# Optimization experiments

Hardware: AMD Instinct MI355X
Metric: run time of the kernel (lower is better)

## Reference

```python
import jax, jax.numpy as jnp
import numpy as np

B, L, D, H, F = 4, 1024, 1024, 16, 4096
HD = D // H
EPS = 1e-5


def _xavier(key, shape):
    fan_in, fan_out = shape[1], shape[0]
    a = np.sqrt(6.0 / (fan_in + fan_out)).astype(np.float32)
    return jax.random.uniform(key, shape, jnp.float32, -a, a)


def setup_inputs() -> dict:
    key = jax.random.key(0)
    ks = jax.random.split(key, 8)
    x = jax.random.normal(ks[0], (B, L, D), jnp.float32)
    attn_mask = jnp.zeros((L, L), jnp.float32)
    return {
        "x": x,
        "attn_mask": attn_mask,
        "in_proj_w": _xavier(ks[1], (3 * D, D)),
        "in_proj_b": jnp.zeros((3 * D,), jnp.float32),
        "out_proj_w": _xavier(ks[2], (D, D)),
        "out_proj_b": jnp.zeros((D,), jnp.float32),
        "lin1_w": _xavier(ks[3], (F, D)),
        "lin1_b": jnp.zeros((F,), jnp.float32),
        "lin2_w": _xavier(ks[4], (D, F)),
        "lin2_b": jnp.zeros((D,), jnp.float32),
        "ln1_g": jnp.ones((D,), jnp.float32),
        "ln1_b": jnp.zeros((D,), jnp.float32),
        "ln2_g": jnp.ones((D,), jnp.float32),
        "ln2_b": jnp.zeros((D,), jnp.float32),
    }


def _layernorm(x, g, b):
    mu = jnp.mean(x, axis=-1, keepdims=True)
    var = jnp.mean(jnp.square(x - mu), axis=-1, keepdims=True)
    return (x - mu) * jax.lax.rsqrt(var + EPS) * g + b


def reference(x, attn_mask, in_proj_w, in_proj_b, out_proj_w, out_proj_b,
              lin1_w, lin1_b, lin2_w, lin2_b, ln1_g, ln1_b, ln2_g, ln2_b):
    # --- self-attention (need_weights=True, average_attn_weights=False) ---
    qkv = x @ in_proj_w.T + in_proj_b          # [B,L,3D]
    q, k, v = jnp.split(qkv, 3, axis=-1)
    q = q.reshape(B, L, H, HD).transpose(0, 2, 1, 3)  # [B,H,L,hd]
    k = k.reshape(B, L, H, HD).transpose(0, 2, 1, 3)
    v = v.reshape(B, L, H, HD).transpose(0, 2, 1, 3)
    scores = jnp.einsum('bhqd,bhkd->bhqk', q, k) / np.sqrt(HD).astype(np.float32)
    scores = scores + attn_mask                # additive [L,L] mask
    attn_w = jax.nn.softmax(scores, axis=-1)   # [B,H,L,L] materialized weights
    ctx = jnp.einsum('bhqk,bhkd->bhqd', attn_w, v)
    ctx = ctx.transpose(0, 2, 1, 3).reshape(B, L, D)
    attn_out = ctx @ out_proj_w.T + out_proj_b
    # --- norm_first=False residual blocks ---
    x = _layernorm(x + attn_out, ln1_g, ln1_b)
    ff = jax.nn.relu(x @ lin1_w.T + lin1_b) @ lin2_w.T + lin2_b
    x = _layernorm(x + ff, ln2_g, ln2_b)
    return (x, attn_w)
```

## Files before the change

### kernel.cpp

```cpp
#include <hip/hip_runtime.h>

#define Bq 4
#define Lq 1024
#define Dq 1024
#define Hq 16
#define HDq 64
#define Fq 4096
#define Mq (Bq*Lq)

typedef unsigned short u16;
using short8  = __attribute__((ext_vector_type(8))) short;
using floatx4 = __attribute__((ext_vector_type(4))) float;

__device__ __forceinline__ float b2f(u16 u) {
  union { unsigned int i; float f; } v; v.i = ((unsigned int)u) << 16; return v.f;
}
__device__ __forceinline__ u16 f2b(float f) {
  union { float f; unsigned int i; } v; v.f = f;
  unsigned int x = v.i;
  unsigned int r = x + 0x7fffu + ((x >> 16) & 1u);
  return (u16)(r >> 16);
}

__device__ __forceinline__ void split2(float v, u16& hi, u16& lo) {
  hi = f2b(v);
  lo = f2b(v - b2f(hi));
}

__device__ __forceinline__ void gl_lds16(const u16* g, u16* l) {
  __builtin_amdgcn_global_load_lds(
      (const __attribute__((address_space(1))) void*)g,
      (__attribute__((address_space(3))) void*)l, 16, 0, 0);
}

__launch_bounds__(256)
__global__ void cvt_f32_bf16(const float* __restrict__ s, u16* __restrict__ d, int n4) {
  const int i = (blockIdx.x * 256 + threadIdx.x) * 4;
  if (i < n4) {
    float4 v = *(const float4*)(s + i);
    ushort4 o;
    o.x = f2b(v.x); o.y = f2b(v.y); o.z = f2b(v.z); o.w = f2b(v.w);
    *(ushort4*)(d + i) = o;
  }
}

template<bool RELU, typename OutT>
__launch_bounds__(256)
__global__ void gemm_bt(const u16* __restrict__ A, int lda,
                        const u16* __restrict__ B, int ldb,
                        const float* __restrict__ bias,
                        OutT* __restrict__ C, int ldc,
                        int K) {
  __shared__ __align__(16) u16 As[128 * 32];
  __shared__ __align__(16) u16 Bs[128 * 32];
  const int tid  = threadIdx.x;
  const int m0   = blockIdx.y * 128;
  const int n0   = blockIdx.x * 128;
  const int lane = tid & 63;
  const int wave = tid >> 6;
  const int wm   = (wave >> 1) * 64;
  const int wn   = (wave & 1) * 64;
  const int lrow = lane & 15;
  const int lk   = (lane >> 4) * 8;

  const int c0 = tid, c1 = tid + 256;
  const int ar0 = c0 >> 2, ac0 = (c0 & 3) * 8;
  const int ar1 = c1 >> 2, ac1 = (c1 & 3) * 8;

  floatx4 acc[4][4] = {};

  for (int k0 = 0; k0 < K; k0 += 32) {
    gl_lds16(A + (size_t)(m0 + ar0) * lda + k0 + ac0, &As[c0 * 8]);
    gl_lds16(A + (size_t)(m0 + ar1) * lda + k0 + ac1, &As[c1 * 8]);
    gl_lds16(B + (size_t)(n0 + ar0) * ldb + k0 + ac0, &Bs[c0 * 8]);
    gl_lds16(B + (size_t)(n0 + ar1) * ldb + k0 + ac1, &Bs[c1 * 8]);
    __syncthreads();

    short8 af[4], bf[4];
#pragma unroll
    for (int t = 0; t < 4; ++t) {
      af[t] = *(const short8*)&As[(wm + t * 16 + lrow) * 32 + lk];
      bf[t] = *(const short8*)&Bs[(wn + t * 16 + lrow) * 32 + lk];
    }
#pragma unroll
    for (int i = 0; i < 4; ++i)
#pragma unroll
      for (int j = 0; j < 4; ++j)
        acc[i][j] = __builtin_amdgcn_mfma_f32_16x16x32_bf16(af[i], bf[j], acc[i][j], 0, 0, 0);
    __syncthreads();
  }

#pragma unroll
  for (int i = 0; i < 4; ++i) {
    const int row = m0 + wm + i * 16 + (lane >> 4) * 4;
#pragma unroll
    for (int j = 0; j < 4; ++j) {
      const int col = n0 + wn + j * 16 + lrow;
      const float bv = bias[col];
#pragma unroll
      for (int r = 0; r < 4; ++r) {
        float v = acc[i][j][r] + bv;
        if (RELU) v = v > 0.f ? v : 0.f;
        if constexpr (sizeof(OutT) == 4) C[(size_t)(row + r) * ldc + col] = v;
        else                             C[(size_t)(row + r) * ldc + col] = f2b(v);
      }
    }
  }
}

__launch_bounds__(256)
__global__ void transpose_v(const float* __restrict__ qkv, u16* __restrict__ vt) {
  __shared__ __align__(16) float t[64][65];
  const int kt = blockIdx.x;
  const int h  = blockIdx.y;
  const int b  = blockIdx.z;
  const int tid = threadIdx.x;
#pragma unroll
  for (int i = 0; i < 16; ++i) {
    int e = i * 256 + tid;
    int kk = e >> 6, d = e & 63;
    t[kk][d] = qkv[((size_t)(b * Lq + kt * 64 + kk)) * (3 * Dq) + 2 * Dq + h * HDq + d];
  }
  __syncthreads();
#pragma unroll
  for (int i = 0; i < 16; ++i) {
    int e = i * 256 + tid;
    int drow = e >> 6, kcol = e & 63;
    vt[(((size_t)(b * Hq + h)) * HDq + drow) * Lq + kt * 64 + kcol] = f2b(t[kcol][drow]);
  }
}

__launch_bounds__(256)
__global__ void split_k(const float* __restrict__ qkv,
                        u16* __restrict__ kh, u16* __restrict__ kl) {
  const int gid = blockIdx.x * 256 + threadIdx.x;
  const int oct = gid & 7;
  const int l   = (gid >> 3) & 1023;
  const int h   = (gid >> 13) & 15;
  const int b   = gid >> 17;
  const float* src = qkv + ((size_t)(b * Lq + l)) * (3 * Dq) + Dq + h * HDq + oct * 8;
  float4 a = *(const float4*)src;
  float4 c = *(const float4*)(src + 4);
  float v[8] = {a.x, a.y, a.z, a.w, c.x, c.y, c.z, c.w};
  short8 hi, lo;
#pragma unroll
  for (int j = 0; j < 8; ++j) {
    u16 hh, ll; split2(v[j], hh, ll);
    hi[j] = (short)hh; lo[j] = (short)ll;
  }
  const size_t off = (((size_t)(b * Hq + h)) * Lq + l) * HDq + oct * 8;
  *(short8*)(kh + off) = hi;
  *(short8*)(kl + off) = lo;
}

__device__ __forceinline__ int ps_idx(int row, int col) {
  return row * 1024 + ((((col >> 3) ^ (row & 7)) << 3) | (col & 7));
}

__device__ __forceinline__ void load_split8(const float* p, short8& hi, short8& lo) {
  float4 a = *(const float4*)p;
  float4 b = *(const float4*)(p + 4);
  float v[8] = {a.x, a.y, a.z, a.w, b.x, b.y, b.z, b.w};
#pragma unroll
  for (int j = 0; j < 8; ++j) {
    u16 h, l; split2(v[j], h, l);
    hi[j] = (short)h; lo[j] = (short)l;
  }
}

__launch_bounds__(512, 4)
__global__ void attn_kernel(const float* __restrict__ qkv,
                            const u16* __restrict__ kh,
                            const u16* __restrict__ kl,
                            const u16* __restrict__ vt,
                            const float* __restrict__ mask,
                            float* __restrict__ attn_w,
                            u16* __restrict__ ctx) {
  __shared__ __align__(16) u16 Ps[16 * 1024];
  __shared__ float redmax[8][16];
  __shared__ float redsum[8][16];
  __shared__ float Pp[4][16][17];

  int lid = (int)blockIdx.x + ((int)blockIdx.y << 6) + ((int)blockIdx.z << 10);
  lid = (lid & 7) * 512 + (lid >> 3);
  const int qt = lid & 63, h = (lid >> 6) & 15, b = lid >> 10;
  const int bh = b * Hq + h;
  const int tid  = threadIdx.x;
  const int lane = tid & 63, wave = tid >> 6;
  const int lrow = lane & 15, quad = lane >> 4;
  const int q0 = qt * 16;

  const float* qbase = qkv + ((size_t)(b * Lq + q0 + lrow)) * (3 * Dq) + h * HDq + quad * 8;
  short8 aqh0, aql0, aqh1, aql1;
  load_split8(qbase,      aqh0, aql0);
  load_split8(qbase + 32, aqh1, aql1);

  const u16* khb = kh + ((size_t)bh * Lq) * HDq + quad * 8;
  const u16* klb = kl + ((size_t)bh * Lq) * HDq + quad * 8;
  floatx4 sc[8];
#pragma unroll
  for (int i = 0; i < 8; ++i) {
    const int n0 = wave * 128 + i * 16;
    const u16* kbh = khb + (size_t)(n0 + lrow) * HDq;
    const u16* kbl = klb + (size_t)(n0 + lrow) * HDq;
    short8 k0h = *(const short8*)kbh;
    short8 k1h = *(const short8*)(kbh + 32);
    short8 k0l = *(const short8*)kbl;
    short8 k1l = *(const short8*)(kbl + 32);
    floatx4 s = {};
    s = __builtin_amdgcn_mfma_f32_16x16x32_bf16(aqh0, k0h, s, 0, 0, 0);
    s = __builtin_amdgcn_mfma_f32_16x16x32_bf16(aqh0, k0l, s, 0, 0, 0);
    s = __builtin_amdgcn_mfma_f32_16x16x32_bf16(aql0, k0h, s, 0, 0, 0);
    s = __builtin_amdgcn_mfma_f32_16x16x32_bf16(aqh1, k1h, s, 0, 0, 0);
    s = __builtin_amdgcn_mfma_f32_16x16x32_bf16(aqh1, k1l, s, 0, 0, 0);
    s = __builtin_amdgcn_mfma_f32_16x16x32_bf16(aql1, k1h, s, 0, 0, 0);
    sc[i] = s;
  }

  const float* mbase = mask + (size_t)(q0 + quad * 4) * Lq + wave * 128 + lrow;
  float mx[4] = {-1e30f, -1e30f, -1e30f, -1e30f};
#pragma unroll
  for (int i = 0; i < 8; ++i)
#pragma unroll
    for (int r = 0; r < 4; ++r) {
      float v = sc[i][r] * 0.125f + mbase[(size_t)r * Lq + i * 16];
      sc[i][r] = v;
      mx[r] = fmaxf(mx[r], v);
    }
#pragma unroll
  for (int s = 1; s < 16; s <<= 1)
#pragma unroll
    for (int r = 0; r < 4; ++r) mx[r] = fmaxf(mx[r], __shfl_xor(mx[r], s, 16));
  if (lrow == 0) {
#pragma unroll
    for (int r = 0; r < 4; ++r) redmax[wave][quad * 4 + r] = mx[r];
  }
  __syncthreads();
  float M[4];
#pragma unroll
  for (int r = 0; r < 4; ++r) {
    float m = redmax[0][quad * 4 + r];
#pragma unroll
    for (int w = 1; w < 8; ++w) m = fmaxf(m, redmax[w][quad * 4 + r]);
    M[r] = m;
  }

  float sm[4] = {0.f, 0.f, 0.f, 0.f};
#pragma unroll
  for (int i = 0; i < 8; ++i)
#pragma unroll
    for (int r = 0; r < 4; ++r) {
      float p = __expf(sc[i][r] - M[r]);
      sc[i][r] = p;
      sm[r] += p;
    }
#pragma unroll
  for (int s = 1; s < 16; s <<= 1)
#pragma unroll
    for (int r = 0; r < 4; ++r) sm[r] += __shfl_xor(sm[r], s, 16);
  if (lrow == 0) {
#pragma unroll
    for (int r = 0; r < 4; ++r) redsum[wave][quad * 4 + r] = sm[r];
  }
  __syncthreads();
  float scl[4];
#pragma unroll
  for (int r = 0; r < 4; ++r) {
    float t = redsum[0][quad * 4 + r];
#pragma unroll
    for (int w = 1; w < 8; ++w) t += redsum[w][quad * 4 + r];
    scl[r] = 1.f / t;
  }

  float* wbase = attn_w + ((size_t)bh * Lq + q0 + quad * 4) * Lq + wave * 128 + lrow;
#pragma unroll
  for (int i = 0; i < 8; ++i)
#pragma unroll
    for (int r = 0; r < 4; ++r) {
      float w = sc[i][r] * scl[r];
      wbase[(size_t)r * Lq + i * 16] = w;
      Ps[ps_idx(quad * 4 + r, wave * 128 + i * 16 + lrow)] = f2b(w);
    }
  __syncthreads();

  const int dstrip = (wave & 3) * 16;
  const int khalf  = (wave >> 2) * 512;
  const u16* vbase = vt + ((size_t)bh * HDq + dstrip + lrow) * Lq + khalf + quad * 8;
  floatx4 o = {};
#pragma unroll
  for (int kc = 0; kc < 512; kc += 32) {
    short8 ap = *(const short8*)&Ps[ps_idx(lrow, khalf + kc + quad * 8)];
    short8 bv = *(const short8*)(vbase + kc);
    o = __builtin_amdgcn_mfma_f32_16x16x32_bf16(ap, bv, o, 0, 0, 0);
  }
  if (wave >= 4) {
#pragma unroll
    for (int r = 0; r < 4; ++r) Pp[wave - 4][quad * 4 + r][lrow] = o[r];
  }
  __syncthreads();
  if (wave < 4) {
#pragma unroll
    for (int r = 0; r < 4; ++r) {
      float v = o[r] + Pp[wave][quad * 4 + r][lrow];
      ctx[((size_t)(b * Lq) + q0 + quad * 4 + r) * Dq + h * HDq + dstrip + lrow] = f2b(v);
    }
  }
}

template<typename OutT>
__launch_bounds__(256)
__global__ void add_ln(const u16* __restrict__ a, const u16* __restrict__ res,
                       const float* __restrict__ g, const float* __restrict__ be,
                       OutT* __restrict__ out) {
  const int rowi = blockIdx.x;
  const int tid = threadIdx.x;
  const u16* pa = a   + (size_t)rowi * Dq + tid * 4;
  const u16* pr = res + (size_t)rowi * Dq + tid * 4;
  ushort4 va = *(const ushort4*)pa;
  ushort4 vr = *(const ushort4*)pr;
  float v[4];
  float s = 0.f, s2 = 0.f;
#pragma unroll
  for (int j = 0; j < 4; ++j) {
    float x = b2f(((const u16*)&va)[j]) + b2f(((const u16*)&vr)[j]);
    v[j] = x; s += x; s2 += x * x;
  }
#pragma unroll
  for (int m = 1; m < 64; m <<= 1) { s += __shfl_xor(s, m, 64); s2 += __shfl_xor(s2, m, 64); }
  __shared__ float rs[4], rs2[4];
  const int wave = tid >> 6, lane = tid & 63;
  if (lane == 0) { rs[wave] = s; rs2[wave] = s2; }
  __syncthreads();
  s  = rs[0] + rs[1] + rs[2] + rs[3];
  s2 = rs2[0] + rs2[1] + rs2[2] + rs2[3];
  const float mean = s * (1.f / Dq);
  const float var  = s2 * (1.f / Dq) - mean * mean;
  const float rstd = rsqrtf(var + 1e-5f);
  float4 vg = *(const float4*)(g + tid * 4);
  float4 vb = *(const float4*)(be + tid * 4);
  float y0 = (v[0] - mean) * rstd * vg.x + vb.x;
  float y1 = (v[1] - mean) * rstd * vg.y + vb.y;
  float y2 = (v[2] - mean) * rstd * vg.z + vb.z;
  float y3 = (v[3] - mean) * rstd * vg.w + vb.w;
  if constexpr (sizeof(OutT) == 4) {
    float4 o = {y0, y1, y2, y3};
    *(float4*)(out + (size_t)rowi * Dq + tid * 4) = o;
  } else {
    ushort4 o;
    ((u16*)&o)[0] = f2b(y0); ((u16*)&o)[1] = f2b(y1);
    ((u16*)&o)[2] = f2b(y2); ((u16*)&o)[3] = f2b(y3);
    *(ushort4*)(out + (size_t)rowi * Dq + tid * 4) = o;
  }
}

extern "C" void kernel_launch(void* const* d_in, const int* in_sizes, int n_in,
                              void* d_out, int out_size, void* d_ws, size_t ws_size,
                              hipStream_t stream) {
  const float* x    = (const float*)d_in[0];
  const float* mask = (const float*)d_in[1];
  const float* win  = (const float*)d_in[2];
  const float* bin  = (const float*)d_in[3];
  const float* wo   = (const float*)d_in[4];
  const float* bo   = (const float*)d_in[5];
  const float* w1   = (const float*)d_in[6];
  const float* b1   = (const float*)d_in[7];
  const float* w2   = (const float*)d_in[8];
  const float* b2   = (const float*)d_in[9];
  const float* g1   = (const float*)d_in[10];
  const float* be1  = (const float*)d_in[11];
  const float* g2   = (const float*)d_in[12];
  const float* be2  = (const float*)d_in[13];

  float* out0  = (float*)d_out;
  float* attnw = out0 + (size_t)Bq * Lq * Dq;

  u16*   ws   = (u16*)d_ws;
  u16*   xb   = ws;
  float* qkvf = (float*)(ws + (size_t)4194304);
  u16*   vtb  = ws + (size_t)29360128;
  u16*   ctx  = ws + (size_t)33554432;
  u16*   aout = ws + (size_t)37748736;
  u16*   winb = ws + (size_t)41943040;
  u16*   wob  = ws + (size_t)45088768;
  u16*   w1b  = ws + (size_t)46137344;
  u16*   w2b  = ws + (size_t)50331648;
  u16*   y1   = aout;
  u16*   h1   = ws + (size_t)4194304;
  u16*   ff   = ctx;
  u16*   khb  = w1b;
  u16*   klb  = w2b;

  cvt_f32_bf16<<<4194304 / 1024, 256, 0, stream>>>(x,   xb,   4194304);
  cvt_f32_bf16<<<3145728 / 1024, 256, 0, stream>>>(win, winb, 3145728);

  gemm_bt<false, float><<<dim3(3 * Dq / 128, Mq / 128), 256, 0, stream>>>(
      xb, Dq, winb, Dq, bin, qkvf, 3 * Dq, Dq);
  transpose_v<<<dim3(16, Hq, Bq), 256, 0, stream>>>(qkvf, vtb);
  split_k<<<524288 / 256, 256, 0, stream>>>(qkvf, khb, klb);
  attn_kernel<<<dim3(Lq / 16, Hq, Bq), 512, 0, stream>>>(qkvf, khb, klb, vtb, mask, attnw, ctx);
  cvt_f32_bf16<<<1048576 / 1024, 256, 0, stream>>>(wo,  wob,  1048576);
  cvt_f32_bf16<<<4194304 / 1024, 256, 0, stream>>>(w1,  w1b,  4194304);
  cvt_f32_bf16<<<4194304 / 1024, 256, 0, stream>>>(w2,  w2b,  4194304);
  gemm_bt<false, u16><<<dim3(Dq / 128, Mq / 128), 256, 0, stream>>>(
      ctx, Dq, wob, Dq, bo, aout, Dq, Dq);
  add_ln<u16><<<Mq, 256, 0, stream>>>(xb, aout, g1, be1, y1);
  gemm_bt<true, u16><<<dim3(Fq / 128, Mq / 128), 256, 0, stream>>>(
      y1, Dq, w1b, Dq, b1, h1, Fq, Dq);
  gemm_bt<false, u16><<<dim3(Dq / 128, Mq / 128), 256, 0, stream>>>(
      h1, Fq, w2b, Fq, b2, ff, Dq, Fq);
  add_ln<float><<<Mq, 256, 0, stream>>>(y1, ff, g2, be2, out0);
}
```

Before: 765.0 us.

## Split-K the out-proj and FFN2 GEMMs and fuse the partial reduction into LayerNorm

The out_proj and lin2 GEMMs now use a two-way split-K kernel. Each half of K writes an fp32 partial tile to its own buffer, which doubles the grid from 256 to 512 blocks so the CUs are better filled. Summing the partials and adding the bias now happens in the residual+LayerNorm kernel, which removes the separate bf16 GEMM output and its epilogue. In the attention kernel, the global stores of the attention weights are moved after the LDS barrier so they can overlap with the PV MFMA loop. The cost is extra fp32 partial traffic and new workspace aliasing that must not collide with live buffers.

```diff
diff --git a/kernel.cpp b/kernel.cpp
--- a/kernel.cpp
+++ b/kernel.cpp
@@ -108,6 +108,69 @@
   }
 }
 
+template<int KS>
+__launch_bounds__(256)
+__global__ void gemm_bt_ks(const u16* __restrict__ A, int lda,
+                           const u16* __restrict__ B, int ldb,
+                           float* __restrict__ P0, float* __restrict__ P1,
+                           int ldc) {
+  __shared__ __align__(16) u16 As[128 * 32];
+  __shared__ __align__(16) u16 Bs[128 * 32];
+  const int z = blockIdx.z;
+  A += (size_t)z * KS;
+  B += (size_t)z * KS;
+  float* C = z ? P1 : P0;
+
+  const int tid  = threadIdx.x;
+  const int m0   = blockIdx.y * 128;
+  const int n0   = blockIdx.x * 128;
+  const int lane = tid & 63;
+  const int wave = tid >> 6;
+  const int wm   = (wave >> 1) * 64;
+  const int wn   = (wave & 1) * 64;
+  const int lrow = lane & 15;
+  const int lk   = (lane >> 4) * 8;
+
+  const int c0 = tid, c1 = tid + 256;
+  const int ar0 = c0 >> 2, ac0 = (c0 & 3) * 8;
+  const int ar1 = c1 >> 2, ac1 = (c1 & 3) * 8;
+
+  floatx4 acc[4][4] = {};
+
+  for (int k0 = 0; k0 < KS; k0 += 32) {
+    gl_lds16(A + (size_t)(m0 + ar0) * lda + k0 + ac0, &As[c0 * 8]);
+    gl_lds16(A + (size_t)(m0 + ar1) * lda + k0 + ac1, &As[c1 * 8]);
+    gl_lds16(B + (size_t)(n0 + ar0) * ldb + k0 + ac0, &Bs[c0 * 8]);
+    gl_lds16(B + (size_t)(n0 + ar1) * ldb + k0 + ac1, &Bs[c1 * 8]);
+    __syncthreads();
+
+    short8 af[4], bf[4];
+#pragma unroll
+    for (int t = 0; t < 4; ++t) {
+      af[t] = *(const short8*)&As[(wm + t * 16 + lrow) * 32 + lk];
+      bf[t] = *(const short8*)&Bs[(wn + t * 16 + lrow) * 32 + lk];
+    }
+#pragma unroll
+    for (int i = 0; i < 4; ++i)
+#pragma unroll
+      for (int j = 0; j < 4; ++j)
+        acc[i][j] = __builtin_amdgcn_mfma_f32_16x16x32_bf16(af[i], bf[j], acc[i][j], 0, 0, 0);
+    __syncthreads();
+  }
+
+#pragma unroll
+  for (int i = 0; i < 4; ++i) {
+    const int row = m0 + wm + i * 16 + (lane >> 4) * 4;
+#pragma unroll
+    for (int j = 0; j < 4; ++j) {
+      const int col = n0 + wn + j * 16 + lrow;
+#pragma unroll
+      for (int r = 0; r < 4; ++r)
+        C[(size_t)(row + r) * ldc + col] = acc[i][j][r];
+    }
+  }
+}
+
 __launch_bounds__(256)
 __global__ void transpose_v(const float* __restrict__ qkv, u16* __restrict__ vt) {
   __shared__ __align__(16) float t[64][65];
@@ -272,16 +335,22 @@
     scl[r] = 1.f / t;
   }
 
-  float* wbase = attn_w + ((size_t)bh * Lq + q0 + quad * 4) * Lq + wave * 128 + lrow;
 #pragma unroll
   for (int i = 0; i < 8; ++i)
 #pragma unroll
     for (int r = 0; r < 4; ++r) {
       float w = sc[i][r] * scl[r];
-      wbase[(size_t)r * Lq + i * 16] = w;
+      sc[i][r] = w;
       Ps[ps_idx(quad * 4 + r, wave * 128 + i * 16 + lrow)] = f2b(w);
     }
   __syncthreads();
+
+  float* wbase = attn_w + ((size_t)bh * Lq + q0 + quad * 4) * Lq + wave * 128 + lrow;
+#pragma unroll
+  for (int i = 0; i < 8; ++i)
+#pragma unroll
+    for (int r = 0; r < 4; ++r)
+      wbase[(size_t)r * Lq + i * 16] = sc[i][r];
 
   const int dstrip = (wave & 3) * 16;
   const int khalf  = (wave >> 2) * 512;
@@ -309,22 +378,27 @@
 
 template<typename OutT>
 __launch_bounds__(256)
-__global__ void add_ln(const u16* __restrict__ a, const u16* __restrict__ res,
-                       const float* __restrict__ g, const float* __restrict__ be,
-                       OutT* __restrict__ out) {
+__global__ void add_ln_red(const u16* __restrict__ res,
+                           const float* __restrict__ p0,
+                           const float* __restrict__ p1,
+                           const float* __restrict__ bias,
+                           const float* __restrict__ g, const float* __restrict__ be,
+                           OutT* __restrict__ out) {
   const int rowi = blockIdx.x;
   const int tid = threadIdx.x;
-  const u16* pa = a   + (size_t)rowi * Dq + tid * 4;
-  const u16* pr = res + (size_t)rowi * Dq + tid * 4;
-  ushort4 va = *(const ushort4*)pa;
-  ushort4 vr = *(const ushort4*)pr;
+  const size_t off = (size_t)rowi * Dq + tid * 4;
+  ushort4 vr = *(const ushort4*)(res + off);
+  float4 a0 = *(const float4*)(p0 + off);
+  float4 a1 = *(const float4*)(p1 + off);
+  float4 bb = *(const float4*)(bias + tid * 4);
   float v[4];
+  v[0] = b2f(vr.x) + a0.x + a1.x + bb.x;
+  v[1] = b2f(vr.y) + a0.y + a1.y + bb.y;
+  v[2] = b2f(vr.z) + a0.z + a1.z + bb.z;
+  v[3] = b2f(vr.w) + a0.w + a1.w + bb.w;
   float s = 0.f, s2 = 0.f;
 #pragma unroll
-  for (int j = 0; j < 4; ++j) {
-    float x = b2f(((const u16*)&va)[j]) + b2f(((const u16*)&vr)[j]);
-    v[j] = x; s += x; s2 += x * x;
-  }
+  for (int j = 0; j < 4; ++j) { s += v[j]; s2 += v[j] * v[j]; }
 #pragma unroll
   for (int m = 1; m < 64; m <<= 1) { s += __shfl_xor(s, m, 64); s2 += __shfl_xor(s2, m, 64); }
   __shared__ float rs[4], rs2[4];
@@ -344,12 +418,12 @@
   float y3 = (v[3] - mean) * rstd * vg.w + vb.w;
   if constexpr (sizeof(OutT) == 4) {
     float4 o = {y0, y1, y2, y3};
-    *(float4*)(out + (size_t)rowi * Dq + tid * 4) = o;
+    *(float4*)(out + off) = o;
   } else {
     ushort4 o;
     ((u16*)&o)[0] = f2b(y0); ((u16*)&o)[1] = f2b(y1);
     ((u16*)&o)[2] = f2b(y2); ((u16*)&o)[3] = f2b(y3);
-    *(ushort4*)(out + (size_t)rowi * Dq + tid * 4) = o;
+    *(ushort4*)(out + off) = o;
   }
 }
 
@@ -386,9 +460,12 @@
   u16*   w2b  = ws + (size_t)50331648;
   u16*   y1   = aout;
   u16*   h1   = ws + (size_t)4194304;
-  u16*   ff   = ctx;
   u16*   khb  = w1b;
   u16*   klb  = w2b;
+  float* poA = (float*)(ws + (size_t)4194304);
+  float* poB = (float*)(ws + (size_t)12582912);
+  float* plA = (float*)(ws + (size_t)20971520);
+  float* plB = (float*)(ws + (size_t)29360128);
 
   cvt_f32_bf16<<<4194304 / 1024, 256, 0, stream>>>(x,   xb,   4194304);
   cvt_f32_bf16<<<3145728 / 1024, 256, 0, stream>>>(win, winb, 3145728);
@@ -401,12 +478,12 @@
   cvt_f32_bf16<<<1048576 / 1024, 256, 0, stream>>>(wo,  wob,  1048576);
   cvt_f32_bf16<<<4194304 / 1024, 256, 0, stream>>>(w1,  w1b,  4194304);
   cvt_f32_bf16<<<4194304 / 1024, 256, 0, stream>>>(w2,  w2b,  4194304);
-  gemm_bt<false, u16><<<dim3(Dq / 128, Mq / 128), 256, 0, stream>>>(
-      ctx, Dq, wob, Dq, bo, aout, Dq, Dq);
-  add_ln<u16><<<Mq, 256, 0, stream>>>(xb, aout, g1, be1, y1);
+  gemm_bt_ks<512><<<dim3(Dq / 128, Mq / 128, 2), 256, 0, stream>>>(
+      ctx, Dq, wob, Dq, poA, poB, Dq);
+  add_ln_red<u16><<<Mq, 256, 0, stream>>>(xb, poA, poB, bo, g1, be1, y1);
   gemm_bt<true, u16><<<dim3(Fq / 128, Mq / 128), 256, 0, stream>>>(
       y1, Dq, w1b, Dq, b1, h1, Fq, Dq);
-  gemm_bt<false, u16><<<dim3(Dq / 128, Mq / 128), 256, 0, stream>>>(
-      h1, Fq, w2b, Fq, b2, ff, Dq, Fq);
-  add_ln<float><<<Mq, 256, 0, stream>>>(y1, ff, g2, be2, out0);
-}
+  gemm_bt_ks<2048><<<dim3(Dq / 128, Mq / 128, 2), 256, 0, stream>>>(
+      h1, Fq, w2b, Fq, plA, plB, Dq);
+  add_ln_red<float><<<Mq, 256, 0, stream>>>(y1, plA, plB, b2, g2, be2, out0);
+}
```

Result: faster. 732.4 us (-4.3%).
